# Optimization experiments

Measured on AMD Instinct MI355X. Metric: run time of the kernel, lower is better.

Reference implementation:

```python
import jax, jax.numpy as jnp
import numpy as np

N_ATOMS = 10000
N_PAIRS = 320000
C = 64        # channel width (pp_nodes[-1], ii_nodes[-1], pi_nodes[-1])
NB = 10       # n_basis
EPS = 1e-3    # torsion-boost epsilon


def setup_inputs() -> dict:
    key = jax.random.key(0)
    ks = jax.random.split(key, 24)
    f32 = jnp.float32

    def w(k, shp):
        return jax.random.normal(k, shp, f32) / np.float32(np.sqrt(shp[0]))

    ind_2 = jax.random.randint(ks[0], (N_PAIRS, 2), 0, N_ATOMS)
    p1 = jax.random.normal(ks[1], (N_ATOMS, C), f32)
    p3 = jax.random.normal(ks[2], (N_ATOMS, 3, C), f32)
    basis = jax.random.uniform(ks[3], (N_PAIRS, NB), dtype=f32)
    d3 = jax.random.normal(ks[4], (N_PAIRS, 3), f32)
    d3 = d3 / jnp.linalg.norm(d3, axis=-1, keepdims=True)  # unit bond directions
    fc_edge = jax.random.uniform(ks[5], (N_PAIRS, 1), dtype=f32)  # cutoff in [0,1]

    return {
        'ind_2': ind_2, 'p1': p1, 'p3': p3, 'basis': basis, 'd3': d3, 'fc_edge': fc_edge,
        'pp_pre_W1': w(ks[6], (C, C)), 'pp_pre_b1': jnp.zeros((C,), f32),
        'pp_pre_W2': w(ks[7], (C, C)), 'pp_pre_b2': jnp.zeros((C,), f32),
        'pi_W': w(ks[8], (2 * C, C * NB)), 'pi_b': jnp.zeros((C * NB,), f32),
        'ii_W': w(ks[9], (C, 2 * C)),
        'pp_post_W1': w(ks[10], (2 * C, C)), 'pp_post_W2': w(ks[11], (C, C)),
        'eq_pp_W': w(ks[12], (C, C)),
        'pp1_W1': w(ks[13], (2 * C, C)), 'pp1_b1': jnp.zeros((C,), f32),
        'pp1_W2': w(ks[14], (C, 2 * C)), 'pp1_b2': jnp.zeros((2 * C,), f32),
    }


def _gc_block(ind_2, p1, p3, basis, d3, fc_edge,
              pp_pre_W1, pp_pre_b1, pp_pre_W2, pp_pre_b2,
              pi_W, pi_b, ii_W, pp_post_W1, pp_post_W2,
              eq_pp_W, pp1_W1, pp1_b1, pp1_W2, pp1_b2):
    n_atoms = p1.shape[0]
    i = ind_2[:, 0]
    j = ind_2[:, 1]

    # ---- InvarLayer ----
    # pp_pre: FF [C,C], tanh, bias
    p1_in = jnp.tanh(jnp.tanh(p1 @ pp_pre_W1 + pp_pre_b1) @ pp_pre_W2 + pp_pre_b2)
    # PILayer: concat(p1[i], p1[j]) -> Dense(C*NB) -> contract with radial basis
    pair = jnp.concatenate([p1_in[i], p1_in[j]], axis=-1)            # (P, 2C)
    h = jnp.tanh(pair @ pi_W + pi_b).reshape(-1, C, NB)              # (P, C, NB)
    i_pair = jnp.einsum('pcb,pb->pc', h, basis)                      # (P, C)
    # ii: FF [2C] (doubled for n_props=2), tanh, no bias
    i_pair = jnp.tanh(i_pair @ ii_W)                                 # (P, 2C)
    # IP: scatter-add onto receiver atom i
    p1_scat = jax.ops.segment_sum(i_pair, i, num_segments=n_atoms)   # (N, 2C)
    # pp_post: FF [C,C], tanh, no bias
    p1_new = jnp.tanh(jnp.tanh(p1_scat @ pp_post_W1) @ pp_post_W2)   # (N, C)

    i1a, i1b = jnp.split(i_pair, 2, axis=-1)  # chunks; rank-3 branch uses i1s[1]

    # ---- torsion boost (compute_torsion_boost_t3) ----
    v = jax.ops.segment_sum(d3 * fc_edge, i, num_segments=n_atoms)   # (N, 3)
    v_i = v[i]
    proj = jnp.sum(v_i * d3, axis=-1, keepdims=True)
    w = v_i - proj * d3                                              # perpendicular part
    w2 = jnp.sum(w * w, axis=-1, keepdims=True)
    g_deg = w2 / (w2 + (10.0 * EPS) ** 2)
    t3 = w * jax.lax.rsqrt(w2 + EPS * EPS) * g_deg                   # (P, 3)
    tb_gate = g_deg * (fc_edge * fc_edge)                            # (P, 1)

    # ---- EquivarLayer ----
    gate = i1b[:, None, :]                                           # (P, 1, C)
    ix = p3[j] * gate + d3[:, :, None] * gate \
         + t3[:, :, None] * (i1b * tb_gate)[:, None, :]              # (P, 3, C)
    p3_new = jax.ops.segment_sum(ix, i, num_segments=n_atoms)        # (N, 3, C)
    p3_new = p3_new @ eq_pp_W                                        # PP: no bias, no act
    dotted = jnp.einsum('ixr,ixr->ir', p3_new, p3_new)               # (N, C)

    # ---- output PP + gating ----
    h2 = jnp.tanh(jnp.concatenate([p1_new, dotted], axis=-1) @ pp1_W1 + pp1_b1)
    h2 = jnp.tanh(h2 @ pp1_W2 + pp1_b2)                              # (N, 2C)
    g1, g3 = jnp.split(h2, 2, axis=-1)
    p1_out = g1                                                      # (N, C)
    p3_out = p3_new * g3[:, None, :]                                 # ScaleLayer
    return p1_out, p3_out


def reference(ind_2, p1, p3, basis, d3, fc_edge,
              pp_pre_W1, pp_pre_b1, pp_pre_W2, pp_pre_b2,
              pi_W, pi_b, ii_W, pp_post_W1, pp_post_W2,
              eq_pp_W, pp1_W1, pp1_b1, pp1_W2, pp1_b2):
    return _gc_block(ind_2, p1, p3, basis, d3, fc_edge,
                     pp_pre_W1, pp_pre_b1, pp_pre_W2, pp_pre_b2,
                     pi_W, pi_b, ii_W, pp_post_W1, pp_post_W2,
                     eq_pp_W, pp1_W1, pp1_b1, pp1_W2, pp1_b2)
```

## Files before the change

kernel.cpp:

```cpp
#include <hip/hip_runtime.h>
#include <hip/hip_bf16.h>

#define N_ATOMS 10000
#define N_PAIRS 320000
#define C_ 64
#define NB_ 10

typedef short bf16x8 __attribute__((ext_vector_type(8)));
typedef float f32x4 __attribute__((ext_vector_type(4)));

__device__ __forceinline__ float bf2f(__hip_bfloat16 x) { return __bfloat162float(x); }
__device__ __forceinline__ float ldf(const void* p, int i, int isf32) {
    return isf32 ? ((const float*)p)[i] : bf2f(((const __hip_bfloat16*)p)[i]);
}
__device__ __forceinline__ short f2bs(float x) {
    __hip_bfloat16 h = __float2bfloat16(x);
    return *reinterpret_cast<short*>(&h);
}
__device__ __forceinline__ float bs2f(unsigned short s) {
    return __uint_as_float(((unsigned)s) << 16);
}
__device__ __forceinline__ float tanh_fast(float x) {
    const float e = __expf(2.0f * x);
    return 1.0f - 2.0f * __builtin_amdgcn_rcpf(e + 1.0f);
}

#define W_PPREW1 0
#define W_PPREB1 4096
#define W_PPREW2 4160
#define W_PPREB2 8256
#define W_PIW    8320
#define W_PIB    90240
#define W_IIW    90880
#define W_PPOSTW1 99072
#define W_PPOSTW2 107264
#define W_EQW    111360
#define W_Q1W    115456
#define W_Q1B    123648
#define W_Q2W    123712
#define W_Q2B    131904
#define W_TOTAL  132032

__global__ void k_probe(const void* __restrict__ d3, int* __restrict__ flag)
{
    if (threadIdx.x == 0 && blockIdx.x == 0) {
        float sf = 0.f, sb = 0.f;
        const float* f = (const float*)d3;
        const __hip_bfloat16* b = (const __hip_bfloat16*)d3;
        for (int r = 0; r < 4; r++) {
            float x = f[r*3], y = f[r*3+1], z = f[r*3+2];
            float n = x*x + y*y + z*z;
            sf += isfinite(n) ? fabsf(n - 1.f) : 1e30f;
            float xb = bf2f(b[r*3]), yb = bf2f(b[r*3+1]), zb = bf2f(b[r*3+2]);
            float nb = xb*xb + yb*yb + zb*zb;
            sb += isfinite(nb) ? fabsf(nb - 1.f) : 1e30f;
        }
        *flag = (sf < sb) ? 1 : 0;
    }
}

__global__ __launch_bounds__(256) void k_convert(
    const void* s0, const void* s1, const void* s2, const void* s3,
    const void* s4, const void* s5, const void* s6, const void* s7,
    const void* s8, const void* s9, const void* s10, const void* s11,
    const void* s12, const void* s13,
    float* __restrict__ wbuf, const int* __restrict__ flagp)
{
    const int idx = blockIdx.x * 256 + threadIdx.x;
    if (idx >= W_TOTAL) return;
    const int isf32 = *flagp;
    const int offs[15] = {W_PPREW1, W_PPREB1, W_PPREW2, W_PPREB2, W_PIW, W_PIB,
                          W_IIW, W_PPOSTW1, W_PPOSTW2, W_EQW, W_Q1W, W_Q1B,
                          W_Q2W, W_Q2B, W_TOTAL};
    const void* srcs[14] = {s0,s1,s2,s3,s4,s5,s6,s7,s8,s9,s10,s11,s12,s13};
    int t = 0;
    while (idx >= offs[t + 1]) t++;
    wbuf[idx] = ldf(srcs[t], idx - offs[t], isf32);
}

__global__ __launch_bounds__(256) void k_pack(
    const float* __restrict__ wbuf,
    short* __restrict__ piWBh, short* __restrict__ piWBl,
    short* __restrict__ iiWh, short* __restrict__ iiWl)
{
    int idx = blockIdx.x * 256 + threadIdx.x;
    if (idx < 81920) {
        const int j = idx & 7, lane = (idx >> 3) & 63, s = (idx >> 9) & 3, T = idx >> 11;
        const int k = s * 32 + (lane >> 4) * 8 + j;
        const int colp = T * 16 + (lane & 15);
        const int b = colp >> 6, c = colp & 63;
        const float v = wbuf[W_PIW + k * 640 + c * 10 + b];
        const short hs = f2bs(v);
        piWBh[idx] = hs;
        piWBl[idx] = f2bs(v - bs2f((unsigned short)hs));
        return;
    }
    idx -= 81920;
    if (idx < 8192) {
        const int j = idx & 7, lane = (idx >> 3) & 63, s2 = (idx >> 9) & 1, ct = idx >> 10;
        const int k = s2 * 32 + (lane >> 4) * 8 + j;
        const int col = ct * 16 + (lane & 15);
        const float wv = wbuf[W_IIW + k * 128 + col];
        const short hs = f2bs(wv);
        iiWh[idx] = hs;
        iiWl[idx] = f2bs(wv - bs2f((unsigned short)hs));
    }
}

__global__ __launch_bounds__(256) void k_p1in(
    const void* __restrict__ p1, const float* __restrict__ wbuf,
    const int* __restrict__ flagp,
    unsigned short* __restrict__ p1h, unsigned short* __restrict__ p1l)
{
    const float* W1 = wbuf + W_PPREW1;
    const float* b1 = wbuf + W_PPREB1;
    const float* W2 = wbuf + W_PPREW2;
    const float* b2 = wbuf + W_PPREB2;
    const int isf32 = *flagp;
    __shared__ float x[4][C_];
    __shared__ float h[4][C_];
    const int t = threadIdx.x;
    const int slot = t >> 6, c = t & 63;
    const int atom = blockIdx.x * 4 + slot;
    x[slot][c] = ldf(p1, atom * C_ + c, isf32);
    __syncthreads();
    float acc = b1[c];
    for (int k = 0; k < C_; k++) acc += x[slot][k] * W1[k * C_ + c];
    h[slot][c] = tanh_fast(acc);
    __syncthreads();
    acc = b2[c];
    for (int k = 0; k < C_; k++) acc += h[slot][k] * W2[k * C_ + c];
    const float f = tanh_fast(acc);
    const short hs = f2bs(f);
    p1h[atom * C_ + c] = (unsigned short)hs;
    p1l[atom * C_ + c] = (unsigned short)f2bs(f - bs2f((unsigned short)hs));
}

__global__ __launch_bounds__(256) void k_hist(const int* __restrict__ ind2, int* __restrict__ cnt)
{
    const int p = blockIdx.x * 256 + threadIdx.x;
    if (p < N_PAIRS) atomicAdd(&cnt[ind2[2 * p]], 1);
}
__global__ __launch_bounds__(256) void k_scan(const int* __restrict__ cnt, int* __restrict__ offs)
{
    __shared__ int part[256];
    __shared__ int base[257];
    const int t = threadIdx.x;
    const int lo = t * 40, hi = (lo + 40 < N_ATOMS) ? lo + 40 : N_ATOMS;
    int s = 0;
    for (int b = lo; b < hi; b++) s += cnt[b];
    part[t] = s;
    __syncthreads();
    if (t == 0) {
        int run = 0;
        for (int i = 0; i < 256; i++) { base[i] = run; run += part[i]; }
        base[256] = run;
    }
    __syncthreads();
    int run = base[t];
    for (int b = lo; b < hi; b++) { offs[b] = run; run += cnt[b]; }
    if (t == 0) offs[N_ATOMS] = base[256];
}
__global__ __launch_bounds__(256) void k_cpcur(const int* __restrict__ offs, int* __restrict__ cur)
{
    const int i = blockIdx.x * 256 + threadIdx.x;
    if (i < N_ATOMS) cur[i] = offs[i];
}
__global__ __launch_bounds__(256) void k_scatter(const int* __restrict__ ind2,
                                                 int* __restrict__ cur, int* __restrict__ perm)
{
    const int p = blockIdx.x * 256 + threadIdx.x;
    if (p >= N_PAIRS) return;
    const int pos = atomicAdd(&cur[ind2[2 * p]], 1);
    perm[pos] = p;
}

__global__ __launch_bounds__(256) void k_vscat(
    const int* __restrict__ ind2, const void* __restrict__ d3,
    const void* __restrict__ fc, const int* __restrict__ flagp,
    const int* __restrict__ perm, float* __restrict__ v)
{
    __shared__ int iA[256];
    __shared__ float sx[256], sy[256], sz[256];
    const int t = threadIdx.x;
    const int q = blockIdx.x * 256 + t;
    const int isf32 = *flagp;
    const int p = perm[q];
    const int ia = ind2[2 * p];
    const float f = ldf(fc, p, isf32);
    iA[t] = ia;
    sx[t] = ldf(d3, 3 * p + 0, isf32) * f;
    sy[t] = ldf(d3, 3 * p + 1, isf32) * f;
    sz[t] = ldf(d3, 3 * p + 2, isf32) * f;
    __syncthreads();
    const bool head = (t == 0) || (iA[t - 1] != ia);
    if (head) {
        float ax = sx[t], ay = sy[t], az = sz[t];
        int m = t + 1;
        while (m < 256 && iA[m] == ia) { ax += sx[m]; ay += sy[m]; az += sz[m]; m++; }
        atomicAdd(&v[ia * 3 + 0], ax);
        atomicAdd(&v[ia * 3 + 1], ay);
        atomicAdd(&v[ia * 3 + 2], az);
    }
}

__global__ __launch_bounds__(256) void k_pairs(
    const int* __restrict__ ind2, const void* __restrict__ basis,
    const void* __restrict__ d3, const void* __restrict__ fc,
    const void* __restrict__ p3,
    const float* __restrict__ wbuf,
    const short* __restrict__ piWBh, const short* __restrict__ piWBl,
    const short* __restrict__ iiWh, const short* __restrict__ iiWl,
    const unsigned short* __restrict__ p1h, const unsigned short* __restrict__ p1l,
    const int* __restrict__ flagp, const float* __restrict__ vglob,
    const int* __restrict__ perm,
    float* __restrict__ p1scat, float* __restrict__ p3acc)
{
    __shared__ __align__(16) char U[33792];
    unsigned short* Bbuf = (unsigned short*)U;
    float* preL = (float*)(U + 16384);
    float* ipL  = (float*)U;
    __shared__ float basisL[640];
    __shared__ int pmL[64], sIL[64], sJL[64];
    __shared__ float fcL[64], d3L[64][3], t3L[64][3], tbL[64];

    const int t = threadIdx.x;
    const int P0 = blockIdx.x * 64;
    const int isf32 = *flagp;
    const int lane = t & 63;
    const int w = t >> 6;
    const int lc = lane & 15;
    const int quad = lane >> 4;

    if (t < 64) pmL[t] = perm[P0 + t];
    __syncthreads();
    if (t < 64) {
        const int p = pmL[t];
        int2 ij = ((const int2*)ind2)[p];
        sIL[t] = ij.x; sJL[t] = ij.y;
        fcL[t] = ldf(fc, p, isf32);
        d3L[t][0] = ldf(d3, 3 * p + 0, isf32);
        d3L[t][1] = ldf(d3, 3 * p + 1, isf32);
        d3L[t][2] = ldf(d3, 3 * p + 2, isf32);
    }
    for (int e = t; e < 640; e += 256) {
        const int m = e / 10, b = e % 10;
        basisL[e] = ldf(basis, pmL[m] * 10 + b, isf32);
    }
    __syncthreads();

    bf16x8 ah[4], al[4];
    {
        const int ia = sIL[w * 16 + lc];
        const int ja = sJL[w * 16 + lc];
        #pragma unroll
        for (int s = 0; s < 4; s++) {
            const int atom = (s < 2) ? ia : ja;
            const int off = atom * 64 + (s & 1) * 32 + quad * 8;
            ah[s] = *(const bf16x8*)(p1h + off);
            al[s] = *(const bf16x8*)(p1l + off);
        }
    }

    float sr[4][4];
    #pragma unroll
    for (int r = 0; r < 4; r++)
        #pragma unroll
        for (int ph = 0; ph < 4; ph++) sr[r][ph] = 0.f;

    for (int cc = 0; cc < 10; cc++) {
        f32x4 acc[4];
        #pragma unroll
        for (int tt = 0; tt < 4; tt++) acc[tt] = (f32x4){0.f, 0.f, 0.f, 0.f};

        __syncthreads();
        {
            const uint4* gsrc = (const uint4*)(piWBh + cc * 8192);
            uint4* ldst = (uint4*)Bbuf;
            #pragma unroll
            for (int r = 0; r < 4; r++) ldst[r * 256 + t] = gsrc[r * 256 + t];
        }
        __syncthreads();
        #pragma unroll
        for (int tt = 0; tt < 4; tt++) {
            #pragma unroll
            for (int s = 0; s < 4; s++) {
                bf16x8 bfr = *(const bf16x8*)&Bbuf[((tt * 4 + s) * 64 + lane) * 8];
                acc[tt] = __builtin_amdgcn_mfma_f32_16x16x32_bf16(ah[s], bfr, acc[tt], 0, 0, 0);
                acc[tt] = __builtin_amdgcn_mfma_f32_16x16x32_bf16(al[s], bfr, acc[tt], 0, 0, 0);
            }
        }
        __syncthreads();
        {
            const uint4* gsrc = (const uint4*)(piWBl + cc * 8192);
            uint4* ldst = (uint4*)Bbuf;
            #pragma unroll
            for (int r = 0; r < 4; r++) ldst[r * 256 + t] = gsrc[r * 256 + t];
        }
        __syncthreads();
        #pragma unroll
        for (int tt = 0; tt < 4; tt++) {
            #pragma unroll
            for (int s = 0; s < 4; s++) {
                bf16x8 bfr = *(const bf16x8*)&Bbuf[((tt * 4 + s) * 64 + lane) * 8];
                acc[tt] = __builtin_amdgcn_mfma_f32_16x16x32_bf16(ah[s], bfr, acc[tt], 0, 0, 0);
            }
            const int c = tt * 16 + lc;
            const float bias = wbuf[W_PIB + c * 10 + cc];
            #pragma unroll
            for (int r = 0; r < 4; r++) {
                const int m = w * 16 + quad * 4 + r;
                const float h = tanh_fast(acc[tt][r] + bias);
                sr[r][tt] += h * basisL[m * 10 + cc];
            }
        }
    }

    __syncthreads();
    #pragma unroll
    for (int r = 0; r < 4; r++)
        #pragma unroll
        for (int ph = 0; ph < 4; ph++)
            preL[(w * 16 + quad * 4 + r) * 68 + ph * 16 + lc] = sr[r][ph];
    __syncthreads();

    bf16x8 ah2[2], al2[2];
    {
        const int row = w * 16 + lc;
        #pragma unroll
        for (int s2 = 0; s2 < 2; s2++) {
            const float* pr2 = &preL[row * 68 + s2 * 32 + quad * 8];
            #pragma unroll
            for (int j = 0; j < 8; j++) {
                const float x = pr2[j];
                const short hs = f2bs(x);
                ah2[s2][j] = hs;
                al2[s2][j] = f2bs(x - bs2f((unsigned short)hs));
            }
        }
    }
    __syncthreads();

    #pragma unroll
    for (int ct = 0; ct < 8; ct++) {
        f32x4 acc = {0.f, 0.f, 0.f, 0.f};
        #pragma unroll
        for (int s2 = 0; s2 < 2; s2++) {
            bf16x8 bh = *(const bf16x8*)&iiWh[((ct * 2 + s2) * 64 + lane) * 8];
            bf16x8 bl = *(const bf16x8*)&iiWl[((ct * 2 + s2) * 64 + lane) * 8];
            acc = __builtin_amdgcn_mfma_f32_16x16x32_bf16(ah2[s2], bh, acc, 0, 0, 0);
            acc = __builtin_amdgcn_mfma_f32_16x16x32_bf16(al2[s2], bh, acc, 0, 0, 0);
            acc = __builtin_amdgcn_mfma_f32_16x16x32_bf16(ah2[s2], bl, acc, 0, 0, 0);
        }
        const int ch = ct * 16 + lc;
        #pragma unroll
        for (int r = 0; r < 4; r++) {
            const int m = w * 16 + quad * 4 + r;
            ipL[m * 132 + ch] = tanh_fast(acc[r]);
        }
    }
    __syncthreads();

    if (t < 64) {
        const int m = t;
        const int ia = sIL[m];
        const float vi0 = vglob[ia * 3 + 0], vi1 = vglob[ia * 3 + 1], vi2 = vglob[ia * 3 + 2];
        const float d0 = d3L[m][0], d1 = d3L[m][1], d2 = d3L[m][2];
        const float proj = vi0 * d0 + vi1 * d1 + vi2 * d2;
        const float w0 = vi0 - proj * d0, w1 = vi1 - proj * d1, w2v = vi2 - proj * d2;
        const float w2 = w0 * w0 + w1 * w1 + w2v * w2v;
        const float g = w2 / (w2 + 1e-4f);
        const float rs = rsqrtf(w2 + 1e-6f);
        t3L[m][0] = w0 * rs * g; t3L[m][1] = w1 * rs * g; t3L[m][2] = w2v * rs * g;
        const float f = fcL[m];
        tbL[m] = g * f * f;
    }

    {
        const int ch = t & 127;
        const int m0 = (t >> 7) * 32;
        int cur = sIL[m0];
        float acc = 0.f;
        #pragma unroll 4
        for (int m = m0; m < m0 + 32; m++) {
            const int ia = sIL[m];
            if (ia != cur) {
                atomicAdd(&p1scat[(size_t)cur * 128 + ch], acc);
                acc = 0.f; cur = ia;
            }
            acc += ipL[m * 132 + ch];
        }
        atomicAdd(&p1scat[(size_t)cur * 128 + ch], acc);
    }
    __syncthreads();

    if (t < 192) {
        const int x = t >> 6, c = t & 63;
        int cur = sIL[0];
        float acc = 0.f;
        #pragma unroll 4
        for (int m = 0; m < 64; m++) {
            const int ia = sIL[m];
            if (ia != cur) {
                atomicAdd(&p3acc[(size_t)cur * 192 + x * 64 + c], acc);
                acc = 0.f; cur = ia;
            }
            const float bv = ipL[m * 132 + 64 + c];
            const float p3v = ldf(p3, sJL[m] * 192 + x * 64 + c, isf32);
            acc += p3v * bv + d3L[m][x] * bv + t3L[m][x] * (bv * tbL[m]);
        }
        atomicAdd(&p3acc[(size_t)cur * 192 + x * 64 + c], acc);
    }
}

__global__ __launch_bounds__(256) void k_final(
    const float* __restrict__ p1scat, const float* __restrict__ p3acc,
    const float* __restrict__ wbuf, const int* __restrict__ flagp,
    void* __restrict__ out)
{
    const float* ppW1 = wbuf + W_PPOSTW1;
    const float* ppW2 = wbuf + W_PPOSTW2;
    const float* eqW  = wbuf + W_EQW;
    const float* q1W  = wbuf + W_Q1W;
    const float* q1b  = wbuf + W_Q1B;
    const float* q2W  = wbuf + W_Q2W;
    const float* q2b  = wbuf + W_Q2B;
    const int isf32 = *flagp;

    __shared__ float s1[4][128];
    __shared__ float hA[4][64];
    __shared__ float cat[4][128];
    __shared__ float p3a[4][192];
    const int t = threadIdx.x;
    const int slot = t >> 6, c = t & 63;
    const int atom = blockIdx.x * 4 + slot;

    s1[slot][c]        = p1scat[atom * 128 + c];
    s1[slot][64 + c]   = p1scat[atom * 128 + 64 + c];
    p3a[slot][c]       = p3acc[atom * 192 + c];
    p3a[slot][64 + c]  = p3acc[atom * 192 + 64 + c];
    p3a[slot][128 + c] = p3acc[atom * 192 + 128 + c];
    __syncthreads();

    float acc = 0.f;
    for (int k = 0; k < 128; k++) acc += s1[slot][k] * ppW1[k * 64 + c];
    hA[slot][c] = tanh_fast(acc);
    __syncthreads();
    acc = 0.f;
    for (int k = 0; k < 64; k++) acc += hA[slot][k] * ppW2[k * 64 + c];
    cat[slot][c] = tanh_fast(acc);

    float pn[3];
    float dot = 0.f;
    #pragma unroll
    for (int x = 0; x < 3; x++) {
        float a = 0.f;
        for (int k = 0; k < 64; k++) a += p3a[slot][x * 64 + k] * eqW[k * 64 + c];
        pn[x] = a;
        dot += a * a;
    }
    cat[slot][64 + c] = dot;
    __syncthreads();

    acc = q1b[c];
    for (int k = 0; k < 128; k++) acc += cat[slot][k] * q1W[k * 64 + c];
    __syncthreads();
    hA[slot][c] = tanh_fast(acc);
    __syncthreads();

    float g1acc = q2b[c], g3acc = q2b[c + 64];
    for (int k = 0; k < 64; k++) {
        const float hv = hA[slot][k];
        g1acc += hv * q2W[k * 128 + c];
        g3acc += hv * q2W[k * 128 + c + 64];
    }
    const float g1 = tanh_fast(g1acc);
    const float g3 = tanh_fast(g3acc);
    if (isf32) {
        float* p1o = (float*)out;
        float* p3o = p1o + 640000;
        p1o[atom * 64 + c] = g1;
        #pragma unroll
        for (int x = 0; x < 3; x++) p3o[atom * 192 + x * 64 + c] = pn[x] * g3;
    } else {
        __hip_bfloat16* p1o = (__hip_bfloat16*)out;
        __hip_bfloat16* p3o = p1o + 640000;
        p1o[atom * 64 + c] = __float2bfloat16(g1);
        #pragma unroll
        for (int x = 0; x < 3; x++) p3o[atom * 192 + x * 64 + c] = __float2bfloat16(pn[x] * g3);
    }
}

extern "C" void kernel_launch(void* const* d_in, const int* in_sizes, int n_in,
                              void* d_out, int out_size, void* d_ws, size_t ws_size,
                              hipStream_t stream)
{
    const int* ind2 = (const int*)d_in[0];
    const void* p1    = d_in[1];
    const void* p3    = d_in[2];
    const void* basis = d_in[3];
    const void* d3    = d_in[4];
    const void* fc    = d_in[5];

    char* W = (char*)d_ws;
    float* wbuf  = (float*)(W + 0);
    short* piWBh = (short*)(W + 528128);
    short* piWBl = (short*)(W + 691968);
    short* iiWh  = (short*)(W + 855808);
    short* iiWl  = (short*)(W + 872192);
    unsigned short* p1h = (unsigned short*)(W + 888576);
    unsigned short* p1l = (unsigned short*)(W + 2168576);
    int*   flag  = (int*)(W + 3448576);
    int*   cnt   = (int*)(W + 3448640);
    int*   offs  = (int*)(W + 3488640);
    int*   cur   = (int*)(W + 3528704);
    int*   perm  = (int*)(W + 3568704);
    float* v      = (float*)(W + 4848704);
    float* p1scat = (float*)(W + 4968704);
    float* p3acc  = (float*)(W + 10088704);

    hipMemsetAsync(cnt, 0, 40000, stream);
    hipMemsetAsync(v, 0, 120000 + 5120000 + 7680000, stream);

    k_probe<<<1, 64, 0, stream>>>(d3, flag);
    k_convert<<<516, 256, 0, stream>>>(
        d_in[6], d_in[7], d_in[8], d_in[9], d_in[10], d_in[11], d_in[12],
        d_in[13], d_in[14], d_in[15], d_in[16], d_in[17], d_in[18], d_in[19],
        wbuf, flag);
    k_pack<<<352, 256, 0, stream>>>(wbuf, piWBh, piWBl, iiWh, iiWl);
    k_p1in<<<2500, 256, 0, stream>>>(p1, wbuf, flag, p1h, p1l);

    k_hist<<<1250, 256, 0, stream>>>(ind2, cnt);
    k_scan<<<1, 256, 0, stream>>>(cnt, offs);
    k_cpcur<<<40, 256, 0, stream>>>(offs, cur);
    k_scatter<<<1250, 256, 0, stream>>>(ind2, cur, perm);
    k_vscat<<<1250, 256, 0, stream>>>(ind2, d3, fc, flag, perm, v);

    k_pairs<<<5000, 256, 0, stream>>>(ind2, basis, d3, fc, p3,
                                      wbuf, piWBh, piWBl, iiWh, iiWl,
                                      p1h, p1l, flag, v, perm,
                                      p1scat, p3acc);
    k_final<<<2500, 256, 0, stream>>>(p1scat, p3acc, wbuf, flag, d_out);
}
```

Measured before the change: 558.9 us.

## Merge setup kernels, inline dtype probe, stream B from global, stage p3 as fp16

Fuses the probe, weight-convert, pack and p1 pre-MLP kernels into one setup launch and recomputes the dtype probe per block. Folds the cursor copy into the scan and the v-accumulation into the scatter, which now issues per-pair atomics instead of segmented block reductions. In k_pairs the LDS staging of the packed pi weights and its barriers are removed, with B fragments read straight from global memory. p3 is pre-converted to fp16 so the gather is narrower. This cuts launch count and barriers but adds more global B traffic, more atomics and fp16 precision loss on p3.

```diff
diff --git a/kernel.cpp b/kernel.cpp
--- a/kernel.cpp
+++ b/kernel.cpp
@@ -1,5 +1,6 @@
 #include <hip/hip_runtime.h>
 #include <hip/hip_bf16.h>
+#include <hip/hip_fp16.h>
 
 #define N_ATOMS 10000
 #define N_PAIRS 320000
@@ -23,6 +24,21 @@
 __device__ __forceinline__ float tanh_fast(float x) {
     const float e = __expf(2.0f * x);
     return 1.0f - 2.0f * __builtin_amdgcn_rcpf(e + 1.0f);
+}
+__device__ __forceinline__ int probe_isf32(const void* d3) {
+    float sf = 0.f, sb = 0.f;
+    const float* f = (const float*)d3;
+    const __hip_bfloat16* b = (const __hip_bfloat16*)d3;
+    #pragma unroll
+    for (int r = 0; r < 4; r++) {
+        float x = f[r*3], y = f[r*3+1], z = f[r*3+2];
+        float n = x*x + y*y + z*z;
+        sf += isfinite(n) ? fabsf(n - 1.f) : 1e30f;
+        float xb = bf2f(b[r*3]), yb = bf2f(b[r*3+1]), zb = bf2f(b[r*3+2]);
+        float nb = xb*xb + yb*yb + zb*zb;
+        sb += isfinite(nb) ? fabsf(nb - 1.f) : 1e30f;
+    }
+    return (sf < sb) ? 1 : 0;
 }
 
 #define W_PPREW1 0
@@ -41,99 +57,87 @@
 #define W_Q2B    131904
 #define W_TOTAL  132032
 
-__global__ void k_probe(const void* __restrict__ d3, int* __restrict__ flag)
-{
-    if (threadIdx.x == 0 && blockIdx.x == 0) {
-        float sf = 0.f, sb = 0.f;
-        const float* f = (const float*)d3;
-        const __hip_bfloat16* b = (const __hip_bfloat16*)d3;
-        for (int r = 0; r < 4; r++) {
-            float x = f[r*3], y = f[r*3+1], z = f[r*3+2];
-            float n = x*x + y*y + z*z;
-            sf += isfinite(n) ? fabsf(n - 1.f) : 1e30f;
-            float xb = bf2f(b[r*3]), yb = bf2f(b[r*3+1]), zb = bf2f(b[r*3+2]);
-            float nb = xb*xb + yb*yb + zb*zb;
-            sb += isfinite(nb) ? fabsf(nb - 1.f) : 1e30f;
-        }
-        *flag = (sf < sb) ? 1 : 0;
-    }
-}
-
-__global__ __launch_bounds__(256) void k_convert(
+__global__ __launch_bounds__(256) void k_setup(
     const void* s0, const void* s1, const void* s2, const void* s3,
     const void* s4, const void* s5, const void* s6, const void* s7,
     const void* s8, const void* s9, const void* s10, const void* s11,
     const void* s12, const void* s13,
-    float* __restrict__ wbuf, const int* __restrict__ flagp)
-{
-    const int idx = blockIdx.x * 256 + threadIdx.x;
-    if (idx >= W_TOTAL) return;
-    const int isf32 = *flagp;
-    const int offs[15] = {W_PPREW1, W_PPREB1, W_PPREW2, W_PPREB2, W_PIW, W_PIB,
-                          W_IIW, W_PPOSTW1, W_PPOSTW2, W_EQW, W_Q1W, W_Q1B,
-                          W_Q2W, W_Q2B, W_TOTAL};
-    const void* srcs[14] = {s0,s1,s2,s3,s4,s5,s6,s7,s8,s9,s10,s11,s12,s13};
-    int t = 0;
-    while (idx >= offs[t + 1]) t++;
-    wbuf[idx] = ldf(srcs[t], idx - offs[t], isf32);
-}
-
-__global__ __launch_bounds__(256) void k_pack(
-    const float* __restrict__ wbuf,
+    const void* __restrict__ p1, const void* __restrict__ p3,
+    const void* __restrict__ d3,
+    float* __restrict__ wbuf,
     short* __restrict__ piWBh, short* __restrict__ piWBl,
-    short* __restrict__ iiWh, short* __restrict__ iiWl)
-{
-    int idx = blockIdx.x * 256 + threadIdx.x;
-    if (idx < 81920) {
-        const int j = idx & 7, lane = (idx >> 3) & 63, s = (idx >> 9) & 3, T = idx >> 11;
-        const int k = s * 32 + (lane >> 4) * 8 + j;
-        const int colp = T * 16 + (lane & 15);
-        const int b = colp >> 6, c = colp & 63;
-        const float v = wbuf[W_PIW + k * 640 + c * 10 + b];
-        const short hs = f2bs(v);
-        piWBh[idx] = hs;
-        piWBl[idx] = f2bs(v - bs2f((unsigned short)hs));
+    short* __restrict__ iiWh, short* __restrict__ iiWl,
+    __half* __restrict__ p3h16,
+    unsigned short* __restrict__ p1h, unsigned short* __restrict__ p1l)
+{
+    __shared__ int flagS;
+    if (threadIdx.x == 0) flagS = probe_isf32(d3);
+    __syncthreads();
+    const int isf32 = flagS;
+    const int blk = blockIdx.x;
+
+    if (blk < 516) {
+        const int idx = blk * 256 + threadIdx.x;
+        if (idx >= W_TOTAL) return;
+        const int offs[15] = {W_PPREW1, W_PPREB1, W_PPREW2, W_PPREB2, W_PIW, W_PIB,
+                              W_IIW, W_PPOSTW1, W_PPOSTW2, W_EQW, W_Q1W, W_Q1B,
+                              W_Q2W, W_Q2B, W_TOTAL};
+        const void* srcs[14] = {s0,s1,s2,s3,s4,s5,s6,s7,s8,s9,s10,s11,s12,s13};
+        int t = 0;
+        while (idx >= offs[t + 1]) t++;
+        wbuf[idx] = ldf(srcs[t], idx - offs[t], isf32);
         return;
     }
-    idx -= 81920;
-    if (idx < 8192) {
-        const int j = idx & 7, lane = (idx >> 3) & 63, s2 = (idx >> 9) & 1, ct = idx >> 10;
-        const int k = s2 * 32 + (lane >> 4) * 8 + j;
-        const int col = ct * 16 + (lane & 15);
-        const float wv = wbuf[W_IIW + k * 128 + col];
-        const short hs = f2bs(wv);
-        iiWh[idx] = hs;
-        iiWl[idx] = f2bs(wv - bs2f((unsigned short)hs));
-    }
-}
-
-__global__ __launch_bounds__(256) void k_p1in(
-    const void* __restrict__ p1, const float* __restrict__ wbuf,
-    const int* __restrict__ flagp,
-    unsigned short* __restrict__ p1h, unsigned short* __restrict__ p1l)
-{
-    const float* W1 = wbuf + W_PPREW1;
-    const float* b1 = wbuf + W_PPREB1;
-    const float* W2 = wbuf + W_PPREW2;
-    const float* b2 = wbuf + W_PPREB2;
-    const int isf32 = *flagp;
-    __shared__ float x[4][C_];
-    __shared__ float h[4][C_];
-    const int t = threadIdx.x;
-    const int slot = t >> 6, c = t & 63;
-    const int atom = blockIdx.x * 4 + slot;
-    x[slot][c] = ldf(p1, atom * C_ + c, isf32);
-    __syncthreads();
-    float acc = b1[c];
-    for (int k = 0; k < C_; k++) acc += x[slot][k] * W1[k * C_ + c];
-    h[slot][c] = tanh_fast(acc);
-    __syncthreads();
-    acc = b2[c];
-    for (int k = 0; k < C_; k++) acc += h[slot][k] * W2[k * C_ + c];
-    const float f = tanh_fast(acc);
-    const short hs = f2bs(f);
-    p1h[atom * C_ + c] = (unsigned short)hs;
-    p1l[atom * C_ + c] = (unsigned short)f2bs(f - bs2f((unsigned short)hs));
+    if (blk < 868) {
+        int idx = (blk - 516) * 256 + threadIdx.x;
+        if (idx < 81920) {
+            const int j = idx & 7, lane = (idx >> 3) & 63, s = (idx >> 9) & 3, T = idx >> 11;
+            const int k = s * 32 + (lane >> 4) * 8 + j;
+            const int colp = T * 16 + (lane & 15);
+            const int b = colp >> 6, c = colp & 63;
+            const float v = ldf(s4, k * 640 + c * 10 + b, isf32);
+            const short hs = f2bs(v);
+            piWBh[idx] = hs;
+            piWBl[idx] = f2bs(v - bs2f((unsigned short)hs));
+            return;
+        }
+        idx -= 81920;
+        if (idx < 8192) {
+            const int j = idx & 7, lane = (idx >> 3) & 63, s2 = (idx >> 9) & 1, ct = idx >> 10;
+            const int k = s2 * 32 + (lane >> 4) * 8 + j;
+            const int col = ct * 16 + (lane & 15);
+            const float wv = ldf(s6, k * 128 + col, isf32);
+            const short hs = f2bs(wv);
+            iiWh[idx] = hs;
+            iiWl[idx] = f2bs(wv - bs2f((unsigned short)hs));
+        }
+        return;
+    }
+    if (blk < 8368) {
+        const int idx = (blk - 868) * 256 + threadIdx.x;
+        if (idx < N_ATOMS * 192)
+            p3h16[idx] = __float2half(ldf(p3, idx, isf32));
+        return;
+    }
+    {
+        __shared__ float x[4][C_];
+        __shared__ float h[4][C_];
+        const int t = threadIdx.x;
+        const int slot = t >> 6, c = t & 63;
+        const int atom = (blk - 8368) * 4 + slot;
+        x[slot][c] = ldf(p1, atom * C_ + c, isf32);
+        __syncthreads();
+        float acc = ldf(s1, c, isf32);
+        for (int k = 0; k < C_; k++) acc += x[slot][k] * ldf(s0, k * C_ + c, isf32);
+        h[slot][c] = tanh_fast(acc);
+        __syncthreads();
+        acc = ldf(s3, c, isf32);
+        for (int k = 0; k < C_; k++) acc += h[slot][k] * ldf(s2, k * C_ + c, isf32);
+        const float f = tanh_fast(acc);
+        const short hs = f2bs(f);
+        p1h[atom * C_ + c] = (unsigned short)hs;
+        p1l[atom * C_ + c] = (unsigned short)f2bs(f - bs2f((unsigned short)hs));
+    }
 }
 
 __global__ __launch_bounds__(256) void k_hist(const int* __restrict__ ind2, int* __restrict__ cnt)
@@ -141,7 +145,8 @@
     const int p = blockIdx.x * 256 + threadIdx.x;
     if (p < N_PAIRS) atomicAdd(&cnt[ind2[2 * p]], 1);
 }
-__global__ __launch_bounds__(256) void k_scan(const int* __restrict__ cnt, int* __restrict__ offs)
+__global__ __launch_bounds__(256) void k_scan(const int* __restrict__ cnt,
+                                              int* __restrict__ offs, int* __restrict__ cur)
 {
     __shared__ int part[256];
     __shared__ int base[257];
@@ -158,82 +163,60 @@
     }
     __syncthreads();
     int run = base[t];
-    for (int b = lo; b < hi; b++) { offs[b] = run; run += cnt[b]; }
+    for (int b = lo; b < hi; b++) { offs[b] = run; cur[b] = run; run += cnt[b]; }
     if (t == 0) offs[N_ATOMS] = base[256];
 }
-__global__ __launch_bounds__(256) void k_cpcur(const int* __restrict__ offs, int* __restrict__ cur)
-{
-    const int i = blockIdx.x * 256 + threadIdx.x;
-    if (i < N_ATOMS) cur[i] = offs[i];
-}
-__global__ __launch_bounds__(256) void k_scatter(const int* __restrict__ ind2,
-                                                 int* __restrict__ cur, int* __restrict__ perm)
-{
+__global__ __launch_bounds__(256) void k_scatter(
+    const int* __restrict__ ind2, const void* __restrict__ d3,
+    const void* __restrict__ fc,
+    int* __restrict__ cur, int* __restrict__ perm, float* __restrict__ v)
+{
+    __shared__ int flagS;
+    if (threadIdx.x == 0) flagS = probe_isf32(d3);
+    __syncthreads();
+    const int isf32 = flagS;
     const int p = blockIdx.x * 256 + threadIdx.x;
     if (p >= N_PAIRS) return;
-    const int pos = atomicAdd(&cur[ind2[2 * p]], 1);
+    const int ia = ind2[2 * p];
+    const int pos = atomicAdd(&cur[ia], 1);
     perm[pos] = p;
-}
-
-__global__ __launch_bounds__(256) void k_vscat(
-    const int* __restrict__ ind2, const void* __restrict__ d3,
-    const void* __restrict__ fc, const int* __restrict__ flagp,
-    const int* __restrict__ perm, float* __restrict__ v)
-{
-    __shared__ int iA[256];
-    __shared__ float sx[256], sy[256], sz[256];
-    const int t = threadIdx.x;
-    const int q = blockIdx.x * 256 + t;
-    const int isf32 = *flagp;
-    const int p = perm[q];
-    const int ia = ind2[2 * p];
     const float f = ldf(fc, p, isf32);
-    iA[t] = ia;
-    sx[t] = ldf(d3, 3 * p + 0, isf32) * f;
-    sy[t] = ldf(d3, 3 * p + 1, isf32) * f;
-    sz[t] = ldf(d3, 3 * p + 2, isf32) * f;
-    __syncthreads();
-    const bool head = (t == 0) || (iA[t - 1] != ia);
-    if (head) {
-        float ax = sx[t], ay = sy[t], az = sz[t];
-        int m = t + 1;
-        while (m < 256 && iA[m] == ia) { ax += sx[m]; ay += sy[m]; az += sz[m]; m++; }
-        atomicAdd(&v[ia * 3 + 0], ax);
-        atomicAdd(&v[ia * 3 + 1], ay);
-        atomicAdd(&v[ia * 3 + 2], az);
-    }
+    atomicAdd(&v[ia * 3 + 0], ldf(d3, p * 3 + 0, isf32) * f);
+    atomicAdd(&v[ia * 3 + 1], ldf(d3, p * 3 + 1, isf32) * f);
+    atomicAdd(&v[ia * 3 + 2], ldf(d3, p * 3 + 2, isf32) * f);
 }
 
 __global__ __launch_bounds__(256) void k_pairs(
     const int* __restrict__ ind2, const void* __restrict__ basis,
     const void* __restrict__ d3, const void* __restrict__ fc,
-    const void* __restrict__ p3,
+    const __half* __restrict__ p3h,
     const float* __restrict__ wbuf,
     const short* __restrict__ piWBh, const short* __restrict__ piWBl,
     const short* __restrict__ iiWh, const short* __restrict__ iiWl,
     const unsigned short* __restrict__ p1h, const unsigned short* __restrict__ p1l,
-    const int* __restrict__ flagp, const float* __restrict__ vglob,
+    const float* __restrict__ vglob,
     const int* __restrict__ perm,
     float* __restrict__ p1scat, float* __restrict__ p3acc)
 {
     __shared__ __align__(16) char U[33792];
-    unsigned short* Bbuf = (unsigned short*)U;
-    float* preL = (float*)(U + 16384);
+    float* preL = (float*)U;
     float* ipL  = (float*)U;
     __shared__ float basisL[640];
     __shared__ int pmL[64], sIL[64], sJL[64];
     __shared__ float fcL[64], d3L[64][3], t3L[64][3], tbL[64];
+    __shared__ int flagS;
 
     const int t = threadIdx.x;
     const int P0 = blockIdx.x * 64;
-    const int isf32 = *flagp;
     const int lane = t & 63;
     const int w = t >> 6;
     const int lc = lane & 15;
     const int quad = lane >> 4;
 
+    if (t == 0) flagS = probe_isf32(d3);
     if (t < 64) pmL[t] = perm[P0 + t];
     __syncthreads();
+    const int isf32 = flagS;
     if (t < 64) {
         const int p = pmL[t];
         int2 ij = ((const int2*)ind2)[p];
@@ -269,54 +252,31 @@
         for (int ph = 0; ph < 4; ph++) sr[r][ph] = 0.f;
 
     for (int cc = 0; cc < 10; cc++) {
-        f32x4 acc[4];
-        #pragma unroll
-        for (int tt = 0; tt < 4; tt++) acc[tt] = (f32x4){0.f, 0.f, 0.f, 0.f};
-
-        __syncthreads();
-        {
-            const uint4* gsrc = (const uint4*)(piWBh + cc * 8192);
-            uint4* ldst = (uint4*)Bbuf;
-            #pragma unroll
-            for (int r = 0; r < 4; r++) ldst[r * 256 + t] = gsrc[r * 256 + t];
-        }
-        __syncthreads();
+        const short* bh_base = piWBh + cc * 8192;
+        const short* bl_base = piWBl + cc * 8192;
         #pragma unroll
         for (int tt = 0; tt < 4; tt++) {
+            f32x4 acc = {0.f, 0.f, 0.f, 0.f};
             #pragma unroll
             for (int s = 0; s < 4; s++) {
-                bf16x8 bfr = *(const bf16x8*)&Bbuf[((tt * 4 + s) * 64 + lane) * 8];
-                acc[tt] = __builtin_amdgcn_mfma_f32_16x16x32_bf16(ah[s], bfr, acc[tt], 0, 0, 0);
-                acc[tt] = __builtin_amdgcn_mfma_f32_16x16x32_bf16(al[s], bfr, acc[tt], 0, 0, 0);
-            }
-        }
-        __syncthreads();
-        {
-            const uint4* gsrc = (const uint4*)(piWBl + cc * 8192);
-            uint4* ldst = (uint4*)Bbuf;
-            #pragma unroll
-            for (int r = 0; r < 4; r++) ldst[r * 256 + t] = gsrc[r * 256 + t];
-        }
-        __syncthreads();
-        #pragma unroll
-        for (int tt = 0; tt < 4; tt++) {
-            #pragma unroll
-            for (int s = 0; s < 4; s++) {
-                bf16x8 bfr = *(const bf16x8*)&Bbuf[((tt * 4 + s) * 64 + lane) * 8];
-                acc[tt] = __builtin_amdgcn_mfma_f32_16x16x32_bf16(ah[s], bfr, acc[tt], 0, 0, 0);
+                const int fo = ((tt * 4 + s) * 64 + lane) * 8;
+                bf16x8 bh = *(const bf16x8*)(bh_base + fo);
+                bf16x8 bl = *(const bf16x8*)(bl_base + fo);
+                acc = __builtin_amdgcn_mfma_f32_16x16x32_bf16(ah[s], bh, acc, 0, 0, 0);
+                acc = __builtin_amdgcn_mfma_f32_16x16x32_bf16(al[s], bh, acc, 0, 0, 0);
+                acc = __builtin_amdgcn_mfma_f32_16x16x32_bf16(ah[s], bl, acc, 0, 0, 0);
             }
             const int c = tt * 16 + lc;
             const float bias = wbuf[W_PIB + c * 10 + cc];
             #pragma unroll
             for (int r = 0; r < 4; r++) {
                 const int m = w * 16 + quad * 4 + r;
-                const float h = tanh_fast(acc[tt][r] + bias);
+                const float h = tanh_fast(acc[r] + bias);
                 sr[r][tt] += h * basisL[m * 10 + cc];
             }
         }
     }
 
-    __syncthreads();
     #pragma unroll
     for (int r = 0; r < 4; r++)
         #pragma unroll
@@ -406,7 +366,7 @@
                 acc = 0.f; cur = ia;
             }
             const float bv = ipL[m * 132 + 64 + c];
-            const float p3v = ldf(p3, sJL[m] * 192 + x * 64 + c, isf32);
+            const float p3v = __half2float(p3h[sJL[m] * 192 + x * 64 + c]);
             acc += p3v * bv + d3L[m][x] * bv + t3L[m][x] * (bv * tbL[m]);
         }
         atomicAdd(&p3acc[(size_t)cur * 192 + x * 64 + c], acc);
@@ -415,7 +375,7 @@
 
 __global__ __launch_bounds__(256) void k_final(
     const float* __restrict__ p1scat, const float* __restrict__ p3acc,
-    const float* __restrict__ wbuf, const int* __restrict__ flagp,
+    const float* __restrict__ wbuf, const void* __restrict__ d3probe,
     void* __restrict__ out)
 {
     const float* ppW1 = wbuf + W_PPOSTW1;
@@ -425,22 +385,24 @@
     const float* q1b  = wbuf + W_Q1B;
     const float* q2W  = wbuf + W_Q2W;
     const float* q2b  = wbuf + W_Q2B;
-    const int isf32 = *flagp;
 
     __shared__ float s1[4][128];
     __shared__ float hA[4][64];
     __shared__ float cat[4][128];
     __shared__ float p3a[4][192];
+    __shared__ int flagS;
     const int t = threadIdx.x;
     const int slot = t >> 6, c = t & 63;
     const int atom = blockIdx.x * 4 + slot;
 
+    if (t == 0) flagS = probe_isf32(d3probe);
     s1[slot][c]        = p1scat[atom * 128 + c];
     s1[slot][64 + c]   = p1scat[atom * 128 + 64 + c];
     p3a[slot][c]       = p3acc[atom * 192 + c];
     p3a[slot][64 + c]  = p3acc[atom * 192 + 64 + c];
     p3a[slot][128 + c] = p3acc[atom * 192 + 128 + c];
     __syncthreads();
+    const int isf32 = flagS;
 
     float acc = 0.f;
     for (int k = 0; k < 128; k++) acc += s1[slot][k] * ppW1[k * 64 + c];
@@ -510,35 +472,30 @@
     short* iiWl  = (short*)(W + 872192);
     unsigned short* p1h = (unsigned short*)(W + 888576);
     unsigned short* p1l = (unsigned short*)(W + 2168576);
-    int*   flag  = (int*)(W + 3448576);
-    int*   cnt   = (int*)(W + 3448640);
-    int*   offs  = (int*)(W + 3488640);
-    int*   cur   = (int*)(W + 3528704);
-    int*   perm  = (int*)(W + 3568704);
-    float* v      = (float*)(W + 4848704);
-    float* p1scat = (float*)(W + 4968704);
-    float* p3acc  = (float*)(W + 10088704);
+    int*   cnt   = (int*)(W + 3448576);
+    int*   offs  = (int*)(W + 3488576);
+    int*   cur   = (int*)(W + 3528640);
+    int*   perm  = (int*)(W + 3568640);
+    float* v      = (float*)(W + 4848640);
+    float* p1scat = (float*)(W + 4968640);
+    float* p3acc  = (float*)(W + 10088640);
+    __half* p3h = (__half*)(W + 17768640);
 
     hipMemsetAsync(cnt, 0, 40000, stream);
     hipMemsetAsync(v, 0, 120000 + 5120000 + 7680000, stream);
 
-    k_probe<<<1, 64, 0, stream>>>(d3, flag);
-    k_convert<<<516, 256, 0, stream>>>(
+    k_setup<<<10868, 256, 0, stream>>>(
         d_in[6], d_in[7], d_in[8], d_in[9], d_in[10], d_in[11], d_in[12],
         d_in[13], d_in[14], d_in[15], d_in[16], d_in[17], d_in[18], d_in[19],
-        wbuf, flag);
-    k_pack<<<352, 256, 0, stream>>>(wbuf, piWBh, piWBl, iiWh, iiWl);
-    k_p1in<<<2500, 256, 0, stream>>>(p1, wbuf, flag, p1h, p1l);
+        p1, p3, d3, wbuf, piWBh, piWBl, iiWh, iiWl, p3h, p1h, p1l);
 
     k_hist<<<1250, 256, 0, stream>>>(ind2, cnt);
-    k_scan<<<1, 256, 0, stream>>>(cnt, offs);
-    k_cpcur<<<40, 256, 0, stream>>>(offs, cur);
-    k_scatter<<<1250, 256, 0, stream>>>(ind2, cur, perm);
-    k_vscat<<<1250, 256, 0, stream>>>(ind2, d3, fc, flag, perm, v);
-
-    k_pairs<<<5000, 256, 0, stream>>>(ind2, basis, d3, fc, p3,
+    k_scan<<<1, 256, 0, stream>>>(cnt, offs, cur);
+    k_scatter<<<1250, 256, 0, stream>>>(ind2, d3, fc, cur, perm, v);
+
+    k_pairs<<<5000, 256, 0, stream>>>(ind2, basis, d3, fc, p3h,
                                       wbuf, piWBh, piWBl, iiWh, iiWl,
-                                      p1h, p1l, flag, v, perm,
+                                      p1h, p1l, v, perm,
                                       p1scat, p3acc);
-    k_final<<<2500, 256, 0, stream>>>(p1scat, p3acc, wbuf, flag, d_out);
-}
+    k_final<<<2500, 256, 0, stream>>>(p1scat, p3acc, wbuf, d3, d_out);
+}
```

After: 729.0 us. +30.4%, slower.
